# Kernel tuning notes

Hardware: AMD Instinct MI355X
Metric: run time of the kernel (lower is better)

Reference implementation:

```python
import jax, jax.numpy as jnp
import numpy as np
import math

B, S, HID = 1, 2048, 2048
NH, NKV, HD = 32, 8, 64
GROUPS = NH // NKV
BOOST_SCALE, NARROW_SCALE = 1.0, 4.0
NEG = -1e9


def rope_cos_sin(seq_len, scale):
    inv_freq = 1.0 / (10000.0 ** (jnp.arange(0, HD, 2, dtype=jnp.float32) / HD))
    t = jnp.arange(seq_len, dtype=jnp.float32) / scale
    freqs = jnp.outer(t, inv_freq)                      # [s, hd/2]
    emb = jnp.concatenate([freqs, freqs], axis=-1)      # [s, hd]
    return jnp.cos(emb), jnp.sin(emb)


def rotate_half(x):
    x1, x2 = x[..., : HD // 2], x[..., HD // 2:]
    return jnp.concatenate([-x2, x1], axis=-1)


def apply_rope(q, k, cos, sin, position_ids):
    c = cos[position_ids][:, None]                      # [b,1,s,hd]
    s = sin[position_ids][:, None]
    return q * c + rotate_half(q) * s, k * c + rotate_half(k) * s


def setup_inputs() -> dict:
    key = jax.random.key(0)
    ks = jax.random.split(key, 5)
    hidden_states = jax.random.normal(ks[0], (B, S, HID), dtype=jnp.float32)
    i = jnp.arange(S)[:, None]
    j = jnp.arange(S)[None, :]
    attention_mask = jnp.where(j <= i, 0.0, NEG).astype(jnp.float32)[None, None]  # [1,1,S,S]
    position_ids = jnp.broadcast_to(jnp.arange(S, dtype=jnp.int32)[None], (B, S))
    sc = 1.0 / math.sqrt(HID)
    Wq = jax.random.normal(ks[1], (NH * HD, HID), dtype=jnp.float32) * sc
    Wk = jax.random.normal(ks[2], (NKV * HD, HID), dtype=jnp.float32) * sc
    Wv = jax.random.normal(ks[3], (NKV * HD, HID), dtype=jnp.float32) * sc
    Wo = jax.random.normal(ks[4], (HID, HID), dtype=jnp.float32) * sc
    return dict(hidden_states=hidden_states, attention_mask=attention_mask,
                position_ids=position_ids, Wq=Wq, Wk=Wk, Wv=Wv, Wo=Wo)


def reference(hidden_states, attention_mask, position_ids, Wq, Wk, Wv, Wo):
    b, q_len, _ = hidden_states.shape
    kv_seq_len = q_len

    q = (hidden_states @ Wq.T).reshape(b, q_len, NH, HD).transpose(0, 2, 1, 3)   # [b,H,s,hd]
    k = (hidden_states @ Wk.T).reshape(b, q_len, NKV, HD).transpose(0, 2, 1, 3)  # [b,Hkv,s,hd]
    v = (hidden_states @ Wv.T).reshape(b, q_len, NKV, HD).transpose(0, 2, 1, 3)

    boost_cos, boost_sin = rope_cos_sin(kv_seq_len, BOOST_SCALE)
    narrow_cos, narrow_sin = rope_cos_sin(kv_seq_len + 30, NARROW_SCALE)
    bq, bk = apply_rope(q, k, boost_cos, boost_sin, position_ids)
    nq, nk = apply_rope(q, k, narrow_cos, narrow_sin, position_ids)

    # repeat_kv (GQA)
    bk = jnp.repeat(bk, GROUPS, axis=1)
    nk = jnp.repeat(nk, GROUPS, axis=1)
    v = jnp.repeat(v, GROUPS, axis=1)

    inv_sqrt = 1.0 / math.sqrt(HD)
    big = jnp.einsum('bhqd,bhkd->bhqk', bq, bk) * inv_sqrt
    small = jnp.einsum('bhqd,bhkd->bhqk', nq, nk) * inv_sqrt
    big = big + attention_mask
    small = small + attention_mask

    # neighbor mask: tril minus (for rows >= context_length) tril(diag=context_length)
    # which zeroes those rows entirely -> neighbor = (j <= i) & (i < context_length)
    context_length = q_len - 10
    i = jnp.arange(q_len)[:, None]
    j = jnp.arange(kv_seq_len)[None, :]
    neighbor = (j <= i) & (i < context_length)

    merged = jnp.where(neighbor, big, small)
    probs = jax.nn.softmax(merged.astype(jnp.float32), axis=-1).astype(q.dtype)
    attn = jnp.einsum('bhqk,bhkd->bhqd', probs, v)
    attn = attn.transpose(0, 2, 1, 3).reshape(b, q_len, HID)
    return attn @ Wo.T
```

## Files before the change

### kernel.cpp

```cpp
#include <hip/hip_runtime.h>
#include <math.h>

#define S_LEN 2048
#define HIDN  2048
#define NH    32
#define NKV   8
#define HD    64
#define KVW   (NKV * HD)
#define CTX   (S_LEN - 10)

typedef unsigned short u16;
typedef __attribute__((ext_vector_type(4))) float f32x4;
typedef __attribute__((ext_vector_type(16))) float f32x16;
typedef __attribute__((ext_vector_type(8))) short s16x8;

#define QSCL 0.18033688011112042f
#define L2_1E4 13.287712379549449f

__device__ __forceinline__ float bf2f(u16 u) {
  union { unsigned int i; float f; } v; v.i = ((unsigned int)u) << 16; return v.f;
}
__device__ __forceinline__ u16 f2bf(float f) {
  union { float f; unsigned int i; } v; v.f = f;
  unsigned int r = v.i + 0x7fffu + ((v.i >> 16) & 1u);
  return (u16)(r >> 16);
}
__device__ __forceinline__ unsigned int cvt_pk_bf16(float a, float b) {
  unsigned int d;
  asm("v_cvt_pk_bf16_f32 %0, %1, %2" : "=v"(d) : "v"(a), "v"(b));
  return d;
}

__global__ __launch_bounds__(256) void conv_all(
    const float* __restrict__ h,  const float* __restrict__ wq,
    const float* __restrict__ wk, const float* __restrict__ wv,
    const float* __restrict__ wo,
    u16* __restrict__ Hb, u16* __restrict__ Wqb, u16* __restrict__ Wkb,
    u16* __restrict__ Wvb, u16* __restrict__ Wob)
{
  const int i = blockIdx.x * 256 + threadIdx.x;
  const float* src; u16* dst; int off;
  if      (i < 1048576) { src = h;  dst = Hb;  off = i; }
  else if (i < 2097152) { src = wq; dst = Wqb; off = i - 1048576; }
  else if (i < 2359296) { src = wk; dst = Wkb; off = i - 2097152; }
  else if (i < 2621440) { src = wv; dst = Wvb; off = i - 2359296; }
  else                  { src = wo; dst = Wob; off = i - 2621440; }
  const float4 f4 = ((const float4*)src)[off];
  ushort4 o4;
  o4.x = f2bf(f4.x); o4.y = f2bf(f4.y); o4.z = f2bf(f4.z); o4.w = f2bf(f4.w);
  ((ushort4*)dst)[off] = o4;
}

#define BM 128
#define BN 64
#define BK 64

template<int MODE>
__device__ __forceinline__ void gemm_body(
    u16* __restrict__ As, u16* __restrict__ Bs,
    const u16* __restrict__ A, const u16* __restrict__ B,
    void* __restrict__ Cv, void* __restrict__ Cv2,
    int N, int K, int row0, int col0, const int* __restrict__ pos)
{
  const int tid  = threadIdx.x;
  const int wave = tid >> 6;
  const int lane = tid & 63;
  const int l15  = lane & 15;
  const int wr   = wave * 32;

  f32x4 acc[2][4] = {};

  const int srow = wave * 8 + (lane >> 3);
  const int scol = (lane & 7) * 8;

  for (int kt = 0; kt < K; kt += BK) {
#pragma unroll
    for (int it = 0; it < 4; ++it) {
      const u16* gA = A + (size_t)(row0 + it * 32 + srow) * K + kt + scol;
      u16* lA = &As[(it * 32 + wave * 8) * BK];
      __builtin_amdgcn_global_load_lds((const __attribute__((address_space(1))) void*)gA,
                                       (__attribute__((address_space(3))) void*)lA, 16, 0, 0);
    }
#pragma unroll
    for (int it = 0; it < 2; ++it) {
      const u16* gB = B + (size_t)(col0 + it * 32 + srow) * K + kt + scol;
      u16* lB = &Bs[(it * 32 + wave * 8) * BK];
      __builtin_amdgcn_global_load_lds((const __attribute__((address_space(1))) void*)gB,
                                       (__attribute__((address_space(3))) void*)lB, 16, 0, 0);
    }
    __syncthreads();
#pragma unroll
    for (int kk = 0; kk < 2; ++kk) {
      const int ko = kk * 32 + (lane >> 4) * 8;
      s16x8 af[2], bg[4];
#pragma unroll
      for (int mi = 0; mi < 2; ++mi)
        af[mi] = *(const s16x8*)&As[(wr + mi * 16 + l15) * BK + ko];
#pragma unroll
      for (int ni = 0; ni < 4; ++ni)
        bg[ni] = *(const s16x8*)&Bs[(ni * 16 + l15) * BK + ko];
#pragma unroll
      for (int mi = 0; mi < 2; ++mi)
#pragma unroll
        for (int ni = 0; ni < 4; ++ni)
          acc[mi][ni] = __builtin_amdgcn_mfma_f32_16x16x32_bf16(af[mi], bg[ni], acc[mi][ni], 0, 0, 0);
    }
    __syncthreads();
  }

  const int rq = (lane >> 4) * 4;
  const int cq = l15;

  if (MODE == 3) {
#pragma unroll
    for (int mi = 0; mi < 2; ++mi)
#pragma unroll
      for (int ni = 0; ni < 4; ++ni) {
        const int r = row0 + wr + mi * 16 + rq;
        const int c = col0 + ni * 16 + cq;
#pragma unroll
        for (int t = 0; t < 4; ++t)
          ((float*)Cv)[(size_t)(r + t) * N + c] = acc[mi][ni][t];
      }
  } else if (MODE == 2) {
#pragma unroll
    for (int mi = 0; mi < 2; ++mi)
#pragma unroll
      for (int ni = 0; ni < 4; ++ni) {
        const int r = row0 + wr + mi * 16 + rq;
        const int c = col0 + ni * 16 + cq;
        ushort4 o4;
        o4.x = f2bf(acc[mi][ni][0]); o4.y = f2bf(acc[mi][ni][1]);
        o4.z = f2bf(acc[mi][ni][2]); o4.w = f2bf(acc[mi][ni][3]);
        *(ushort4*)&((u16*)Cv)[(size_t)c * S_LEN + r] = o4;
      }
  } else {
#pragma unroll
    for (int mi = 0; mi < 2; ++mi) {
#pragma unroll
      for (int t = 0; t < 4; ++t) {
        const int i = row0 + wr + mi * 16 + rq + t;
        const float fpos = (float)pos[i];
#pragma unroll
        for (int ni = 0; ni < 2; ++ni) {
          const int d = ni * 16 + cq;
          const int c = col0 + d;
          const float f = exp2f(-(float)(2 * d) * (1.0f / HD) * L2_1E4);
          const float x1 = acc[mi][ni][t], x2 = acc[mi][ni + 2][t];
          if (MODE == 0) {
            const float scl = (i < CTX) ? 1.0f : 0.25f;
            const float a  = fpos * scl * f;
            const float cs = __cosf(a), sn = __sinf(a);
            u16* Cq = (u16*)Cv;
            Cq[(size_t)i * N + c]      = f2bf((x1 * cs - x2 * sn) * QSCL);
            Cq[(size_t)i * N + c + 32] = f2bf((x2 * cs + x1 * sn) * QSCL);
          } else {
            const float ab = fpos * f, an = fpos * 0.25f * f;
            const float cb_ = __cosf(ab), sb_ = __sinf(ab);
            const float cn_ = __cosf(an), sn_ = __sinf(an);
            ((u16*)Cv)[(size_t)i * N + c]       = f2bf(x1 * cb_ - x2 * sb_);
            ((u16*)Cv)[(size_t)i * N + c + 32]  = f2bf(x2 * cb_ + x1 * sb_);
            ((u16*)Cv2)[(size_t)i * N + c]      = f2bf(x1 * cn_ - x2 * sn_);
            ((u16*)Cv2)[(size_t)i * N + c + 32] = f2bf(x2 * cn_ + x1 * sn_);
          }
        }
      }
    }
  }
}

__global__ __launch_bounds__(256) void gemm_qkv(
    const u16* __restrict__ A, const u16* __restrict__ Wq, const u16* __restrict__ Wk,
    const u16* __restrict__ Wv, u16* __restrict__ Q, u16* __restrict__ Kb,
    u16* __restrict__ Kn, u16* __restrict__ Vt, const int* __restrict__ pos)
{
  __shared__ u16 As[BM * BK];
  __shared__ u16 Bs[BN * BK];
  const int bn = blockIdx.x;
  const int row0 = blockIdx.y * BM;
  if (bn < 32)
    gemm_body<0>(As, Bs, A, Wq, Q, nullptr, HIDN, HIDN, row0, bn * BN, pos);
  else if (bn < 40)
    gemm_body<1>(As, Bs, A, Wk, Kb, Kn, KVW, HIDN, row0, (bn - 32) * BN, pos);
  else
    gemm_body<2>(As, Bs, A, Wv, Vt, nullptr, KVW, HIDN, row0, (bn - 40) * BN, pos);
}

__global__ __launch_bounds__(256) void gemm_out(
    const u16* __restrict__ A, const u16* __restrict__ B, float* __restrict__ C, int N, int K)
{
  __shared__ u16 As[BM * BK];
  __shared__ u16 Bs[BN * BK];
  gemm_body<3>(As, Bs, A, B, C, nullptr, N, K, blockIdx.y * BM, blockIdx.x * BN, nullptr);
}

#define PAD 8
__global__ __launch_bounds__(256) void attn_mfma(
    const u16* __restrict__ Q, const u16* __restrict__ K, const u16* __restrict__ Kn,
    const u16* __restrict__ Vt, u16* __restrict__ O)
{
  __shared__ __align__(16) u16 Ks[64][HD + PAD];
  __shared__ __align__(16) u16 Kns[64][HD + PAD];
  __shared__ __align__(16) u16 Vts[HD][64 + PAD];
  __shared__ __align__(16) float Of[64][64];
  __shared__ float Lf[2][32];
  __shared__ float Li[2][32];

  const int tid  = threadIdx.x;
  const int wave = tid >> 6;
  const int lane = tid & 63;
  const int l31  = lane & 31;
  const int hi   = lane >> 5;
  const int wr   = wave >> 1;
  const int wk   = wave & 1;
  const int h    = blockIdx.y;
  const int kh   = h >> 2;
  const int pr   = blockIdx.x;

  int sa[2], sb[2];
#pragma unroll
  for (int it = 0; it < 2; ++it) {
    const int u = it * 256 + tid;
    sa[it] = u >> 3;
    sb[it] = (u & 7) * 8;
  }

  for (int ph = 0; ph < 2; ++ph) {
    const int qt = ph ? pr : 31 - pr;
    const int i_base = qt * 64;
    const int rw0 = i_base + wr * 32;
    const bool mixed_blk = (qt == 31);
    const bool mixed_wv  = mixed_blk && (rw0 + 31 >= CTX);

    s16x8 bq[4];
#pragma unroll
    for (int i = 0; i < 4; ++i)
      bq[i] = *(const s16x8*)(Q + (size_t)(rw0 + l31) * HIDN + h * HD + i * 16 + hi * 8);

    f32x16 acc0 = {};
    f32x16 acc1 = {};
    float lsum = 0.f;

    const int ntiles = qt + 1;
    s16x8 kr[2], vr[2], knr[2];
#pragma unroll
    for (int it = 0; it < 2; ++it) {
      kr[it] = *(const s16x8*)(K  + (size_t)sa[it] * KVW + kh * HD + sb[it]);
      vr[it] = *(const s16x8*)(Vt + (size_t)(kh * HD + sa[it]) * S_LEN + sb[it]);
      if (mixed_blk) knr[it] = *(const s16x8*)(Kn + (size_t)sa[it] * KVW + kh * HD + sb[it]);
    }

    for (int t = 0; t < ntiles; ++t) {
      const int jt = t * 64;
      __syncthreads();
#pragma unroll
      for (int it = 0; it < 2; ++it) {
        *(s16x8*)&Ks[sa[it]][sb[it]]  = kr[it];
        *(s16x8*)&Vts[sa[it]][sb[it]] = vr[it];
        if (mixed_blk) *(s16x8*)&Kns[sa[it]][sb[it]] = knr[it];
      }
      __syncthreads();
      if (t + 1 < ntiles) {
        const int jn = jt + 64;
#pragma unroll
        for (int it = 0; it < 2; ++it) {
          kr[it] = *(const s16x8*)(K  + (size_t)(jn + sa[it]) * KVW + kh * HD + sb[it]);
          vr[it] = *(const s16x8*)(Vt + (size_t)(kh * HD + sa[it]) * S_LEN + jn + sb[it]);
          if (mixed_blk) knr[it] = *(const s16x8*)(Kn + (size_t)(jn + sa[it]) * KVW + kh * HD + sb[it]);
        }
      }

      const int j0 = jt + wk * 32;
      if (j0 > rw0 + 31) continue;
      const bool needmask = (j0 + 31 > rw0);

      f32x16 sc = {};
#pragma unroll
      for (int i = 0; i < 4; ++i) {
        const s16x8 ak = *(const s16x8*)&Ks[wk * 32 + l31][i * 16 + hi * 8];
        sc = __builtin_amdgcn_mfma_f32_32x32x16_bf16(ak, bq[i], sc, 0, 0, 0);
      }
      if (mixed_wv) {
        f32x16 scn = {};
#pragma unroll
        for (int i = 0; i < 4; ++i) {
          const s16x8 ak = *(const s16x8*)&Kns[wk * 32 + l31][i * 16 + hi * 8];
          scn = __builtin_amdgcn_mfma_f32_32x32x16_bf16(ak, bq[i], scn, 0, 0, 0);
        }
        const bool nar = (rw0 + l31) >= CTX;
#pragma unroll
        for (int r = 0; r < 16; ++r) sc[r] = nar ? scn[r] : sc[r];
      }

      float p[16];
#pragma unroll
      for (int r = 0; r < 16; ++r) {
        float e = __builtin_amdgcn_exp2f(fminf(sc[r], 80.f));
        if (needmask) {
          const int key = j0 + (r & 3) + 8 * (r >> 2) + 4 * hi;
          e = (key > rw0 + l31) ? 0.f : e;
        }
        p[r] = e;
        lsum += e;
      }

      unsigned int c[4][2];
#pragma unroll
      for (int blk = 0; blk < 4; ++blk) {
        c[blk][0] = cvt_pk_bf16(p[4 * blk + 0], p[4 * blk + 1]);
        c[blk][1] = cvt_pk_bf16(p[4 * blk + 2], p[4 * blk + 3]);
      }

#pragma unroll
      for (int s = 0; s < 2; ++s) {
        unsigned int w0 = c[2 * s][0], w2 = c[2 * s + 1][0];
        unsigned int w1 = c[2 * s][1], w3 = c[2 * s + 1][1];
        asm("v_permlane32_swap_b32 %0, %1" : "+v"(w0), "+v"(w2));
        asm("v_permlane32_swap_b32 %0, %1" : "+v"(w1), "+v"(w3));
        union { unsigned int u[4]; s16x8 v; } af;
        af.u[0] = w0; af.u[1] = w1; af.u[2] = w2; af.u[3] = w3;
        const int kc = wk * 32 + s * 16 + hi * 8;
        const s16x8 v0 = *(const s16x8*)&Vts[l31][kc];
        const s16x8 v1 = *(const s16x8*)&Vts[32 + l31][kc];
        acc0 = __builtin_amdgcn_mfma_f32_32x32x16_bf16(af.v, v0, acc0, 0, 0, 0);
        acc1 = __builtin_amdgcn_mfma_f32_32x32x16_bf16(af.v, v1, acc1, 0, 0, 0);
      }
    }

    lsum += __shfl_xor(lsum, 32, 64);
    __syncthreads();
    if (wk == 1) {
#pragma unroll
      for (int r = 0; r < 16; ++r) {
        const int rl = (r & 3) + 8 * (r >> 2) + 4 * hi;
        Of[wr * 32 + rl][l31]      = acc0[r];
        Of[wr * 32 + rl][l31 + 32] = acc1[r];
      }
      if (hi == 0) Lf[wr][l31] = lsum;
    }
    __syncthreads();
    if (wk == 0) {
      const float tot = lsum + Lf[wr][l31];
      const float inv = 1.0f / fmaxf(tot, 1e-30f);
      if (hi == 0) Li[wr][l31] = inv;
#pragma unroll
      for (int r = 0; r < 16; ++r) {
        const int rl = (r & 3) + 8 * (r >> 2) + 4 * hi;
        const float iv = Li[wr][rl];
        const size_t o = (size_t)(rw0 + rl) * HIDN + h * HD + l31;
        O[o]      = f2bf((acc0[r] + Of[wr * 32 + rl][l31])      * iv);
        O[o + 32] = f2bf((acc1[r] + Of[wr * 32 + rl][l31 + 32]) * iv);
      }
    }
  }
}

extern "C" void kernel_launch(void* const* d_in, const int* in_sizes, int n_in,
                              void* d_out, int out_size, void* d_ws, size_t ws_size,
                              hipStream_t stream)
{
  const float* hidden = (const float*)d_in[0];
  const int* pos      = (const int*)d_in[2];
  const float* Wq = (const float*)d_in[3];
  const float* Wk = (const float*)d_in[4];
  const float* Wv = (const float*)d_in[5];
  const float* Wo = (const float*)d_in[6];
  float* out = (float*)d_out;

  char* ws = (char*)d_ws;
  u16* Qb  = (u16*)(ws);
  u16* Kbb = (u16*)(ws + (8u  << 20));
  u16* Knb = (u16*)(ws + (10u << 20));
  u16* Vtb = (u16*)(ws + (12u << 20));
  u16* Ab  = (u16*)(ws + (14u << 20));
  u16* Hb  = (u16*)(ws + (22u << 20));
  u16* Wqb = (u16*)(ws + (30u << 20));
  u16* Wkb = (u16*)(ws + (38u << 20));
  u16* Wvb = (u16*)(ws + (40u << 20));
  u16* Wob = (u16*)(ws + (42u << 20));

  conv_all<<<dim3(14336), 256, 0, stream>>>(hidden, Wq, Wk, Wv, Wo, Hb, Wqb, Wkb, Wvb, Wob);
  gemm_qkv<<<dim3(48, 16), 256, 0, stream>>>(Hb, Wqb, Wkb, Wvb, Qb, Kbb, Knb, Vtb, pos);
  attn_mfma<<<dim3(16, NH), 256, 0, stream>>>(Qb, Kbb, Knb, Vtb, Ab);
  gemm_out<<<dim3(32, 16), 256, 0, stream>>>(Ab, Wob, out, HIDN, HIDN);
}
```

Baseline: 250.3 us.

## Double-buffer K/V tiles in shared memory to halve barriers in attention loop

Attention kernel now keeps two LDS buffers for the K, narrow-K and V^T tiles. The next tile is written to the alternate buffer while the current one is computed, and global loads are issued two tiles ahead. This leaves one __syncthreads per tile instead of two and overlaps the LDS stores with the MFMA work. In exchange LDS use roughly doubles, which may lower occupancy, and register pressure rises from the deeper prefetch.

New measurement: 252.1 us. No clear change (+0.7%).

```diff
diff --git a/kernel.cpp b/kernel.cpp
--- a/kernel.cpp
+++ b/kernel.cpp
@@ -191,7 +191,7 @@
 {
   __shared__ u16 As[BM * BK];
   __shared__ u16 Bs[BN * BK];
-  gemm_body<3>(As, Bs, A, B, C, nullptr, N, K, blockIdx.y * BM, blockIdx.x * BN, nullptr);
+  gemm_body<3>(As, Bs, A, B, C, nullptr, N, K, blockIdx.y * BM, blockIdx.x * BN, 0);
 }
 
 #define PAD 8
@@ -199,9 +199,9 @@
     const u16* __restrict__ Q, const u16* __restrict__ K, const u16* __restrict__ Kn,
     const u16* __restrict__ Vt, u16* __restrict__ O)
 {
-  __shared__ __align__(16) u16 Ks[64][HD + PAD];
-  __shared__ __align__(16) u16 Kns[64][HD + PAD];
-  __shared__ __align__(16) u16 Vts[HD][64 + PAD];
+  __shared__ __align__(16) u16 Ks[2][64][HD + PAD];
+  __shared__ __align__(16) u16 Kns[2][64][HD + PAD];
+  __shared__ __align__(16) u16 Vts[2][HD][64 + PAD];
   __shared__ __align__(16) float Of[64][64];
   __shared__ float Lf[2][32];
   __shared__ float Li[2][32];
@@ -243,92 +243,97 @@
 
     const int ntiles = qt + 1;
     s16x8 kr[2], vr[2], knr[2];
-#pragma unroll
-    for (int it = 0; it < 2; ++it) {
-      kr[it] = *(const s16x8*)(K  + (size_t)sa[it] * KVW + kh * HD + sb[it]);
-      vr[it] = *(const s16x8*)(Vt + (size_t)(kh * HD + sa[it]) * S_LEN + sb[it]);
-      if (mixed_blk) knr[it] = *(const s16x8*)(Kn + (size_t)sa[it] * KVW + kh * HD + sb[it]);
-    }
+
+    auto LOADT = [&](int tt) {
+      const int jn = tt * 64;
+#pragma unroll
+      for (int it = 0; it < 2; ++it) {
+        kr[it] = *(const s16x8*)(K  + (size_t)(jn + sa[it]) * KVW + kh * HD + sb[it]);
+        vr[it] = *(const s16x8*)(Vt + (size_t)(kh * HD + sa[it]) * S_LEN + jn + sb[it]);
+        if (mixed_blk) knr[it] = *(const s16x8*)(Kn + (size_t)(jn + sa[it]) * KVW + kh * HD + sb[it]);
+      }
+    };
+    auto STORET = [&](int b) {
+#pragma unroll
+      for (int it = 0; it < 2; ++it) {
+        *(s16x8*)&Ks[b][sa[it]][sb[it]]  = kr[it];
+        *(s16x8*)&Vts[b][sa[it]][sb[it]] = vr[it];
+        if (mixed_blk) *(s16x8*)&Kns[b][sa[it]][sb[it]] = knr[it];
+      }
+    };
+
+    LOADT(0);
+    STORET(0);
+    if (ntiles > 1) LOADT(1);
+    __syncthreads();
 
     for (int t = 0; t < ntiles; ++t) {
+      const int cur = t & 1;
+      if (t + 1 < ntiles) STORET(cur ^ 1);
+      if (t + 2 < ntiles) LOADT(t + 2);
+
       const int jt = t * 64;
+      const int j0 = jt + wk * 32;
+      if (j0 <= rw0 + 31) {
+        const bool needmask = (j0 + 31 > rw0);
+
+        f32x16 sc = {};
+#pragma unroll
+        for (int i = 0; i < 4; ++i) {
+          const s16x8 ak = *(const s16x8*)&Ks[cur][wk * 32 + l31][i * 16 + hi * 8];
+          sc = __builtin_amdgcn_mfma_f32_32x32x16_bf16(ak, bq[i], sc, 0, 0, 0);
+        }
+        if (mixed_wv) {
+          f32x16 scn = {};
+#pragma unroll
+          for (int i = 0; i < 4; ++i) {
+            const s16x8 ak = *(const s16x8*)&Kns[cur][wk * 32 + l31][i * 16 + hi * 8];
+            scn = __builtin_amdgcn_mfma_f32_32x32x16_bf16(ak, bq[i], scn, 0, 0, 0);
+          }
+          const bool nar = (rw0 + l31) >= CTX;
+#pragma unroll
+          for (int r = 0; r < 16; ++r) sc[r] = nar ? scn[r] : sc[r];
+        }
+
+        float p[16];
+#pragma unroll
+        for (int r = 0; r < 16; ++r) {
+          float e = __builtin_amdgcn_exp2f(fminf(sc[r], 80.f));
+          if (needmask) {
+            const int key = j0 + (r & 3) + 8 * (r >> 2) + 4 * hi;
+            e = (key > rw0 + l31) ? 0.f : e;
+          }
+          p[r] = e;
+          lsum += e;
+        }
+
+        unsigned int c[4][2];
+#pragma unroll
+        for (int blk = 0; blk < 4; ++blk) {
+          c[blk][0] = cvt_pk_bf16(p[4 * blk + 0], p[4 * blk + 1]);
+          c[blk][1] = cvt_pk_bf16(p[4 * blk + 2], p[4 * blk + 3]);
+        }
+
+#pragma unroll
+        for (int s = 0; s < 2; ++s) {
+          unsigned int w0 = c[2 * s][0], w2 = c[2 * s + 1][0];
+          unsigned int w1 = c[2 * s][1], w3 = c[2 * s + 1][1];
+          asm("v_permlane32_swap_b32 %0, %1" : "+v"(w0), "+v"(w2));
+          asm("v_permlane32_swap_b32 %0, %1" : "+v"(w1), "+v"(w3));
+          union { unsigned int u[4]; s16x8 v; } af;
+          af.u[0] = w0; af.u[1] = w1; af.u[2] = w2; af.u[3] = w3;
+          const int kc = wk * 32 + s * 16 + hi * 8;
+          const s16x8 v0 = *(const s16x8*)&Vts[cur][l31][kc];
+          const s16x8 v1 = *(const s16x8*)&Vts[cur][32 + l31][kc];
+          acc0 = __builtin_amdgcn_mfma_f32_32x32x16_bf16(af.v, v0, acc0, 0, 0, 0);
+          acc1 = __builtin_amdgcn_mfma_f32_32x32x16_bf16(af.v, v1, acc1, 0, 0, 0);
+        }
+      }
+
       __syncthreads();
-#pragma unroll
-      for (int it = 0; it < 2; ++it) {
-        *(s16x8*)&Ks[sa[it]][sb[it]]  = kr[it];
-        *(s16x8*)&Vts[sa[it]][sb[it]] = vr[it];
-        if (mixed_blk) *(s16x8*)&Kns[sa[it]][sb[it]] = knr[it];
-      }
-      __syncthreads();
-      if (t + 1 < ntiles) {
-        const int jn = jt + 64;
-#pragma unroll
-        for (int it = 0; it < 2; ++it) {
-          kr[it] = *(const s16x8*)(K  + (size_t)(jn + sa[it]) * KVW + kh * HD + sb[it]);
-          vr[it] = *(const s16x8*)(Vt + (size_t)(kh * HD + sa[it]) * S_LEN + jn + sb[it]);
-          if (mixed_blk) knr[it] = *(const s16x8*)(Kn + (size_t)(jn + sa[it]) * KVW + kh * HD + sb[it]);
-        }
-      }
-
-      const int j0 = jt + wk * 32;
-      if (j0 > rw0 + 31) continue;
-      const bool needmask = (j0 + 31 > rw0);
-
-      f32x16 sc = {};
-#pragma unroll
-      for (int i = 0; i < 4; ++i) {
-        const s16x8 ak = *(const s16x8*)&Ks[wk * 32 + l31][i * 16 + hi * 8];
-        sc = __builtin_amdgcn_mfma_f32_32x32x16_bf16(ak, bq[i], sc, 0, 0, 0);
-      }
-      if (mixed_wv) {
-        f32x16 scn = {};
-#pragma unroll
-        for (int i = 0; i < 4; ++i) {
-          const s16x8 ak = *(const s16x8*)&Kns[wk * 32 + l31][i * 16 + hi * 8];
-          scn = __builtin_amdgcn_mfma_f32_32x32x16_bf16(ak, bq[i], scn, 0, 0, 0);
-        }
-        const bool nar = (rw0 + l31) >= CTX;
-#pragma unroll
-        for (int r = 0; r < 16; ++r) sc[r] = nar ? scn[r] : sc[r];
-      }
-
-      float p[16];
-#pragma unroll
-      for (int r = 0; r < 16; ++r) {
-        float e = __builtin_amdgcn_exp2f(fminf(sc[r], 80.f));
-        if (needmask) {
-          const int key = j0 + (r & 3) + 8 * (r >> 2) + 4 * hi;
-          e = (key > rw0 + l31) ? 0.f : e;
-        }
-        p[r] = e;
-        lsum += e;
-      }
-
-      unsigned int c[4][2];
-#pragma unroll
-      for (int blk = 0; blk < 4; ++blk) {
-        c[blk][0] = cvt_pk_bf16(p[4 * blk + 0], p[4 * blk + 1]);
-        c[blk][1] = cvt_pk_bf16(p[4 * blk + 2], p[4 * blk + 3]);
-      }
-
-#pragma unroll
-      for (int s = 0; s < 2; ++s) {
-        unsigned int w0 = c[2 * s][0], w2 = c[2 * s + 1][0];
-        unsigned int w1 = c[2 * s][1], w3 = c[2 * s + 1][1];
-        asm("v_permlane32_swap_b32 %0, %1" : "+v"(w0), "+v"(w2));
-        asm("v_permlane32_swap_b32 %0, %1" : "+v"(w1), "+v"(w3));
-        union { unsigned int u[4]; s16x8 v; } af;
-        af.u[0] = w0; af.u[1] = w1; af.u[2] = w2; af.u[3] = w3;
-        const int kc = wk * 32 + s * 16 + hi * 8;
-        const s16x8 v0 = *(const s16x8*)&Vts[l31][kc];
-        const s16x8 v1 = *(const s16x8*)&Vts[32 + l31][kc];
-        acc0 = __builtin_amdgcn_mfma_f32_32x32x16_bf16(af.v, v0, acc0, 0, 0, 0);
-        acc1 = __builtin_amdgcn_mfma_f32_32x32x16_bf16(af.v, v1, acc1, 0, 0, 0);
-      }
     }
 
     lsum += __shfl_xor(lsum, 32, 64);
-    __syncthreads();
     if (wk == 1) {
 #pragma unroll
       for (int r = 0; r < 16; ++r) {
@@ -352,6 +357,7 @@
         O[o + 32] = f2bf((acc1[r] + Of[wr * 32 + rl][l31 + 32]) * iv);
       }
     }
+    __syncthreads();
   }
 }
 
```

## Split paired causal query tiles into separate blocks, load narrow K directly

Applied to the files above, without the earlier changes.

The attention kernel no longer pairs a long and a short causal query tile inside one block. It launches one block per query tile (32 per head), with the longest tiles scheduled first. The narrow-RoPE K tile is now read from global memory only by waves that need it, which removes its shared-memory buffer. Launch bounds now request 4 blocks per CU so more blocks can be resident, at the cost of less balanced per-block work and possible register limits.

After: 301.2 us. 1.2x slower.

```diff
diff --git a/kernel.cpp b/kernel.cpp
--- a/kernel.cpp
+++ b/kernel.cpp
@@ -191,16 +191,15 @@
 {
   __shared__ u16 As[BM * BK];
   __shared__ u16 Bs[BN * BK];
-  gemm_body<3>(As, Bs, A, B, C, nullptr, N, K, blockIdx.y * BM, blockIdx.x * BN, nullptr);
+  gemm_body<3>(As, Bs, A, B, C, nullptr, N, K, blockIdx.y * BM, blockIdx.x * BN, 0);
 }
 
 #define PAD 8
-__global__ __launch_bounds__(256) void attn_mfma(
+__global__ __launch_bounds__(256, 4) void attn_mfma(
     const u16* __restrict__ Q, const u16* __restrict__ K, const u16* __restrict__ Kn,
     const u16* __restrict__ Vt, u16* __restrict__ O)
 {
   __shared__ __align__(16) u16 Ks[64][HD + PAD];
-  __shared__ __align__(16) u16 Kns[64][HD + PAD];
   __shared__ __align__(16) u16 Vts[HD][64 + PAD];
   __shared__ __align__(16) float Of[64][64];
   __shared__ float Lf[2][32];
@@ -215,7 +214,9 @@
   const int wk   = wave & 1;
   const int h    = blockIdx.y;
   const int kh   = h >> 2;
-  const int pr   = blockIdx.x;
+  const int qt   = 31 - (int)blockIdx.x;
+  const int rw0  = qt * 64 + wr * 32;
+  const bool mixed_wv = (qt == 31) && (rw0 + 31 >= CTX);
 
   int sa[2], sb[2];
 #pragma unroll
@@ -225,132 +226,128 @@
     sb[it] = (u & 7) * 8;
   }
 
-  for (int ph = 0; ph < 2; ++ph) {
-    const int qt = ph ? pr : 31 - pr;
-    const int i_base = qt * 64;
-    const int rw0 = i_base + wr * 32;
-    const bool mixed_blk = (qt == 31);
-    const bool mixed_wv  = mixed_blk && (rw0 + 31 >= CTX);
-
-    s16x8 bq[4];
-#pragma unroll
-    for (int i = 0; i < 4; ++i)
-      bq[i] = *(const s16x8*)(Q + (size_t)(rw0 + l31) * HIDN + h * HD + i * 16 + hi * 8);
-
-    f32x16 acc0 = {};
-    f32x16 acc1 = {};
-    float lsum = 0.f;
-
-    const int ntiles = qt + 1;
-    s16x8 kr[2], vr[2], knr[2];
+  s16x8 bq[4];
+#pragma unroll
+  for (int i = 0; i < 4; ++i)
+    bq[i] = *(const s16x8*)(Q + (size_t)(rw0 + l31) * HIDN + h * HD + i * 16 + hi * 8);
+
+  f32x16 acc0 = {};
+  f32x16 acc1 = {};
+  float lsum = 0.f;
+
+  const int ntiles = qt + 1;
+  s16x8 kr[2], vr[2];
+#pragma unroll
+  for (int it = 0; it < 2; ++it) {
+    kr[it] = *(const s16x8*)(K  + (size_t)sa[it] * KVW + kh * HD + sb[it]);
+    vr[it] = *(const s16x8*)(Vt + (size_t)(kh * HD + sa[it]) * S_LEN + sb[it]);
+  }
+
+  const u16* Knp = Kn + (size_t)(wk * 32 + l31) * KVW + kh * HD;
+
+  for (int t = 0; t < ntiles; ++t) {
+    const int jt = t * 64;
+    __syncthreads();
 #pragma unroll
     for (int it = 0; it < 2; ++it) {
-      kr[it] = *(const s16x8*)(K  + (size_t)sa[it] * KVW + kh * HD + sb[it]);
-      vr[it] = *(const s16x8*)(Vt + (size_t)(kh * HD + sa[it]) * S_LEN + sb[it]);
-      if (mixed_blk) knr[it] = *(const s16x8*)(Kn + (size_t)sa[it] * KVW + kh * HD + sb[it]);
-    }
-
-    for (int t = 0; t < ntiles; ++t) {
-      const int jt = t * 64;
-      __syncthreads();
+      *(s16x8*)&Ks[sa[it]][sb[it]]  = kr[it];
+      *(s16x8*)&Vts[sa[it]][sb[it]] = vr[it];
+    }
+    __syncthreads();
+    if (t + 1 < ntiles) {
+      const int jn = jt + 64;
 #pragma unroll
       for (int it = 0; it < 2; ++it) {
-        *(s16x8*)&Ks[sa[it]][sb[it]]  = kr[it];
-        *(s16x8*)&Vts[sa[it]][sb[it]] = vr[it];
-        if (mixed_blk) *(s16x8*)&Kns[sa[it]][sb[it]] = knr[it];
-      }
-      __syncthreads();
-      if (t + 1 < ntiles) {
-        const int jn = jt + 64;
-#pragma unroll
-        for (int it = 0; it < 2; ++it) {
-          kr[it] = *(const s16x8*)(K  + (size_t)(jn + sa[it]) * KVW + kh * HD + sb[it]);
-          vr[it] = *(const s16x8*)(Vt + (size_t)(kh * HD + sa[it]) * S_LEN + jn + sb[it]);
-          if (mixed_blk) knr[it] = *(const s16x8*)(Kn + (size_t)(jn + sa[it]) * KVW + kh * HD + sb[it]);
-        }
-      }
-
-      const int j0 = jt + wk * 32;
-      if (j0 > rw0 + 31) continue;
-      const bool needmask = (j0 + 31 > rw0);
-
-      f32x16 sc = {};
-#pragma unroll
-      for (int i = 0; i < 4; ++i) {
-        const s16x8 ak = *(const s16x8*)&Ks[wk * 32 + l31][i * 16 + hi * 8];
-        sc = __builtin_amdgcn_mfma_f32_32x32x16_bf16(ak, bq[i], sc, 0, 0, 0);
-      }
-      if (mixed_wv) {
-        f32x16 scn = {};
-#pragma unroll
-        for (int i = 0; i < 4; ++i) {
-          const s16x8 ak = *(const s16x8*)&Kns[wk * 32 + l31][i * 16 + hi * 8];
-          scn = __builtin_amdgcn_mfma_f32_32x32x16_bf16(ak, bq[i], scn, 0, 0, 0);
-        }
-        const bool nar = (rw0 + l31) >= CTX;
-#pragma unroll
-        for (int r = 0; r < 16; ++r) sc[r] = nar ? scn[r] : sc[r];
-      }
-
-      float p[16];
-#pragma unroll
-      for (int r = 0; r < 16; ++r) {
-        float e = __builtin_amdgcn_exp2f(fminf(sc[r], 80.f));
-        if (needmask) {
-          const int key = j0 + (r & 3) + 8 * (r >> 2) + 4 * hi;
-          e = (key > rw0 + l31) ? 0.f : e;
-        }
-        p[r] = e;
-        lsum += e;
-      }
-
-      unsigned int c[4][2];
-#pragma unroll
-      for (int blk = 0; blk < 4; ++blk) {
-        c[blk][0] = cvt_pk_bf16(p[4 * blk + 0], p[4 * blk + 1]);
-        c[blk][1] = cvt_pk_bf16(p[4 * blk + 2], p[4 * blk + 3]);
-      }
-
-#pragma unroll
-      for (int s = 0; s < 2; ++s) {
-        unsigned int w0 = c[2 * s][0], w2 = c[2 * s + 1][0];
-        unsigned int w1 = c[2 * s][1], w3 = c[2 * s + 1][1];
-        asm("v_permlane32_swap_b32 %0, %1" : "+v"(w0), "+v"(w2));
-        asm("v_permlane32_swap_b32 %0, %1" : "+v"(w1), "+v"(w3));
-        union { unsigned int u[4]; s16x8 v; } af;
-        af.u[0] = w0; af.u[1] = w1; af.u[2] = w2; af.u[3] = w3;
-        const int kc = wk * 32 + s * 16 + hi * 8;
-        const s16x8 v0 = *(const s16x8*)&Vts[l31][kc];
-        const s16x8 v1 = *(const s16x8*)&Vts[32 + l31][kc];
-        acc0 = __builtin_amdgcn_mfma_f32_32x32x16_bf16(af.v, v0, acc0, 0, 0, 0);
-        acc1 = __builtin_amdgcn_mfma_f32_32x32x16_bf16(af.v, v1, acc1, 0, 0, 0);
-      }
-    }
-
-    lsum += __shfl_xor(lsum, 32, 64);
-    __syncthreads();
-    if (wk == 1) {
-#pragma unroll
-      for (int r = 0; r < 16; ++r) {
-        const int rl = (r & 3) + 8 * (r >> 2) + 4 * hi;
-        Of[wr * 32 + rl][l31]      = acc0[r];
-        Of[wr * 32 + rl][l31 + 32] = acc1[r];
-      }
-      if (hi == 0) Lf[wr][l31] = lsum;
-    }
-    __syncthreads();
-    if (wk == 0) {
-      const float tot = lsum + Lf[wr][l31];
-      const float inv = 1.0f / fmaxf(tot, 1e-30f);
-      if (hi == 0) Li[wr][l31] = inv;
-#pragma unroll
-      for (int r = 0; r < 16; ++r) {
-        const int rl = (r & 3) + 8 * (r >> 2) + 4 * hi;
-        const float iv = Li[wr][rl];
-        const size_t o = (size_t)(rw0 + rl) * HIDN + h * HD + l31;
-        O[o]      = f2bf((acc0[r] + Of[wr * 32 + rl][l31])      * iv);
-        O[o + 32] = f2bf((acc1[r] + Of[wr * 32 + rl][l31 + 32]) * iv);
-      }
+        kr[it] = *(const s16x8*)(K  + (size_t)(jn + sa[it]) * KVW + kh * HD + sb[it]);
+        vr[it] = *(const s16x8*)(Vt + (size_t)(kh * HD + sa[it]) * S_LEN + jn + sb[it]);
+      }
+    }
+
+    const int j0 = jt + wk * 32;
+    if (j0 > rw0 + 31) continue;
+    const bool needmask = (j0 + 31 > rw0);
+
+    s16x8 akn[4];
+    if (mixed_wv) {
+      const u16* p = Knp + (size_t)jt * KVW;
+#pragma unroll
+      for (int i = 0; i < 4; ++i) akn[i] = *(const s16x8*)(p + i * 16 + hi * 8);
+    }
+
+    f32x16 sc = {};
+#pragma unroll
+    for (int i = 0; i < 4; ++i) {
+      const s16x8 ak = *(const s16x8*)&Ks[wk * 32 + l31][i * 16 + hi * 8];
+      sc = __builtin_amdgcn_mfma_f32_32x32x16_bf16(ak, bq[i], sc, 0, 0, 0);
+    }
+    if (mixed_wv) {
+      f32x16 scn = {};
+#pragma unroll
+      for (int i = 0; i < 4; ++i)
+        scn = __builtin_amdgcn_mfma_f32_32x32x16_bf16(akn[i], bq[i], scn, 0, 0, 0);
+      const bool nar = (rw0 + l31) >= CTX;
+#pragma unroll
+      for (int r = 0; r < 16; ++r) sc[r] = nar ? scn[r] : sc[r];
+    }
+
+    float p[16];
+#pragma unroll
+    for (int r = 0; r < 16; ++r) {
+      float e = __builtin_amdgcn_exp2f(fminf(sc[r], 80.f));
+      if (needmask) {
+        const int key = j0 + (r & 3) + 8 * (r >> 2) + 4 * hi;
+        e = (key > rw0 + l31) ? 0.f : e;
+      }
+      p[r] = e;
+      lsum += e;
+    }
+
+    unsigned int c[4][2];
+#pragma unroll
+    for (int blk = 0; blk < 4; ++blk) {
+      c[blk][0] = cvt_pk_bf16(p[4 * blk + 0], p[4 * blk + 1]);
+      c[blk][1] = cvt_pk_bf16(p[4 * blk + 2], p[4 * blk + 3]);
+    }
+
+#pragma unroll
+    for (int s = 0; s < 2; ++s) {
+      unsigned int w0 = c[2 * s][0], w2 = c[2 * s + 1][0];
+      unsigned int w1 = c[2 * s][1], w3 = c[2 * s + 1][1];
+      asm("v_permlane32_swap_b32 %0, %1" : "+v"(w0), "+v"(w2));
+      asm("v_permlane32_swap_b32 %0, %1" : "+v"(w1), "+v"(w3));
+      union { unsigned int u[4]; s16x8 v; } af;
+      af.u[0] = w0; af.u[1] = w1; af.u[2] = w2; af.u[3] = w3;
+      const int kc = wk * 32 + s * 16 + hi * 8;
+      const s16x8 v0 = *(const s16x8*)&Vts[l31][kc];
+      const s16x8 v1 = *(const s16x8*)&Vts[32 + l31][kc];
+      acc0 = __builtin_amdgcn_mfma_f32_32x32x16_bf16(af.v, v0, acc0, 0, 0, 0);
+      acc1 = __builtin_amdgcn_mfma_f32_32x32x16_bf16(af.v, v1, acc1, 0, 0, 0);
+    }
+  }
+
+  lsum += __shfl_xor(lsum, 32, 64);
+  __syncthreads();
+  if (wk == 1) {
+#pragma unroll
+    for (int r = 0; r < 16; ++r) {
+      const int rl = (r & 3) + 8 * (r >> 2) + 4 * hi;
+      Of[wr * 32 + rl][l31]      = acc0[r];
+      Of[wr * 32 + rl][l31 + 32] = acc1[r];
+    }
+    if (hi == 0) Lf[wr][l31] = lsum;
+  }
+  __syncthreads();
+  if (wk == 0) {
+    const float tot = lsum + Lf[wr][l31];
+    const float inv = 1.0f / fmaxf(tot, 1e-30f);
+    if (hi == 0) Li[wr][l31] = inv;
+#pragma unroll
+    for (int r = 0; r < 16; ++r) {
+      const int rl = (r & 3) + 8 * (r >> 2) + 4 * hi;
+      const float iv = Li[wr][rl];
+      const size_t o = (size_t)(rw0 + rl) * HIDN + h * HD + l31;
+      O[o]      = f2bf((acc0[r] + Of[wr * 32 + rl][l31])      * iv);
+      O[o + 32] = f2bf((acc1[r] + Of[wr * 32 + rl][l31 + 32]) * iv);
     }
   }
 }
@@ -381,6 +378,6 @@
 
   conv_all<<<dim3(14336), 256, 0, stream>>>(hidden, Wq, Wk, Wv, Wo, Hb, Wqb, Wkb, Wvb, Wob);
   gemm_qkv<<<dim3(48, 16), 256, 0, stream>>>(Hb, Wqb, Wkb, Wvb, Qb, Kbb, Knb, Vtb, pos);
-  attn_mfma<<<dim3(16, NH), 256, 0, stream>>>(Qb, Kbb, Knb, Vtb, Ab);
+  attn_mfma<<<dim3(32, NH), 256, 0, stream>>>(Qb, Kbb, Knb, Vtb, Ab);
   gemm_out<<<dim3(32, 16), 256, 0, stream>>>(Ab, Wob, out, HIDN, HIDN);
 }
```
